# Kernel tuning notes

Hardware: AMD Instinct MI355X
Metric: run time of the kernel (lower is better)

The kernel has to match this reference:

```python
import jax, jax.numpy as jnp
import numpy as np

B, N, D = 4, 2048, 1024


def setup_inputs() -> dict:
    key = jax.random.key(0)
    ks = jax.random.split(key, 9)
    x = jax.random.normal(ks[0], (B, N, D), dtype=jnp.float32)
    # causal mask: True = masked (set to -inf), per dot_product_attention semantics
    mask = jnp.triu(jnp.ones((N, N), dtype=bool), k=1)
    mask = jnp.broadcast_to(mask, (B, N, N))
    scale = 1.0 / np.sqrt(D)
    Wq = jax.random.normal(ks[1], (D, D), dtype=jnp.float32) * scale
    Wk = jax.random.normal(ks[2], (D, D), dtype=jnp.float32) * scale
    Wv = jax.random.normal(ks[3], (D, D), dtype=jnp.float32) * scale
    Wo = jax.random.normal(ks[4], (D, D), dtype=jnp.float32) * scale
    bq = jnp.zeros((D,), dtype=jnp.float32)
    bk = jnp.zeros((D,), dtype=jnp.float32)
    bv = jnp.zeros((D,), dtype=jnp.float32)
    bo = jnp.zeros((D,), dtype=jnp.float32)
    return {"x": x, "mask": mask, "Wq": Wq, "bq": bq, "Wk": Wk, "bk": bk,
            "Wv": Wv, "bv": bv, "Wo": Wo, "bo": bo}


def reference(x, mask, Wq, bq, Wk, bk, Wv, bv, Wo, bo):
    # QKV projections (single-head despite docstring; module never splits heads)
    Q = x @ Wq + bq  # [b, n, d]
    K = x @ Wk + bk
    V = x @ Wv + bv
    d = K.shape[-1]
    scores = jnp.einsum('bqd,bkd->bqk', Q, K) / jnp.sqrt(jnp.asarray(d, Q.dtype))
    min_infty = jnp.finfo(scores.dtype).min
    scores = jnp.where(mask, min_infty, scores)
    weights = jax.nn.softmax(scores, axis=-1)
    attention = jnp.einsum('bqk,bkd->bqd', weights, V)
    out = attention @ Wo + bo
    return out
```

## Files before the change

kernel.cpp:

```cpp
#include <hip/hip_runtime.h>
#include <hip/hip_bf16.h>

typedef __attribute__((ext_vector_type(8))) short short8;
typedef __attribute__((ext_vector_type(4))) float f32x4;

__device__ inline float b2f(unsigned short u) {
    union { unsigned int i; float f; } c; c.i = ((unsigned int)u) << 16; return c.f;
}
__device__ inline unsigned short f2b(float f) {
    __hip_bfloat16 h = __float2bfloat16(f);
    return *reinterpret_cast<unsigned short*>(&h);
}

__device__ inline void gl_lds16(const unsigned short* g, unsigned short* ldsbase) {
    __builtin_amdgcn_global_load_lds(
        (const __attribute__((address_space(1))) unsigned int*)(g),
        (__attribute__((address_space(3))) unsigned int*)(ldsbase),
        16, 0, 0);
}

__global__ __launch_bounds__(256) void cvt_f32_bf16(
    const float* __restrict__ src, unsigned short* __restrict__ dst, int n4)
{
    int i = blockIdx.x * 256 + threadIdx.x;
    if (i >= n4) return;
    float4 v = ((const float4*)src)[i];
    union { unsigned short u[4]; unsigned long long ll; } p;
    p.u[0] = f2b(v.x); p.u[1] = f2b(v.y); p.u[2] = f2b(v.z); p.u[3] = f2b(v.w);
    ((unsigned long long*)dst)[i] = p.ll;
}

__global__ __launch_bounds__(256) void cvt_transpose(
    const float* __restrict__ src, unsigned short* __restrict__ dst, int R, int C)
{
    __shared__ float tile[32][33];
    const int c0 = blockIdx.x * 32, r0 = blockIdx.y * 32;
    const int tx = threadIdx.x & 31, ty = threadIdx.x >> 5;
    #pragma unroll
    for (int i = ty; i < 32; i += 8)
        tile[i][tx] = src[(long)(r0 + i) * C + c0 + tx];
    __syncthreads();
    #pragma unroll
    for (int i = ty; i < 32; i += 8)
        dst[(long)(c0 + i) * R + r0 + tx] = f2b(tile[tx][i]);
}


#define TILE_DECLS \
    __shared__ __attribute__((aligned(16))) unsigned short As[2 * 128 * 32]; \
    __shared__ __attribute__((aligned(16))) unsigned short Bs[2 * 128 * 32]; \
    const int t = threadIdx.x, lane = t & 63, w = t >> 6; \
    const int wr = w >> 1, wc = w & 1; \
    const int lrow = lane & 15, quad = lane >> 4; \
    f32x4 acc[4][4]; \
    _Pragma("unroll") for (int i = 0; i < 4; i++) \
        _Pragma("unroll") for (int j = 0; j < 4; j++) \
            acc[i][j] = (f32x4){0.f, 0.f, 0.f, 0.f};

#define TILE_KLOOP(gA, lda, gB, ldb, Keff) \
    for (int k0 = 0; k0 < (Keff); k0 += 64) { \
        _Pragma("unroll") for (int p = 0; p < 2; p++) \
            _Pragma("unroll") for (int h = 0; h < 2; h++) { \
                gl_lds16((gA) + (long)h * 16 * (lda) + k0 + p * 32, \
                         &As[p * 4096 + (w * 32 + h * 16) * 32]); \
                gl_lds16((gB) + (long)h * 16 * (ldb) + k0 + p * 32, \
                         &Bs[p * 4096 + (w * 32 + h * 16) * 32]); \
            } \
        __syncthreads(); \
        _Pragma("unroll") for (int p = 0; p < 2; p++) { \
            short8 af[4], bfr[4]; \
            _Pragma("unroll") for (int mi = 0; mi < 4; mi++) \
                af[mi] = *(const short8*)&As[p * 4096 + (wr * 64 + mi * 16 + lrow) * 32 + quad * 8]; \
            _Pragma("unroll") for (int ni = 0; ni < 4; ni++) \
                bfr[ni] = *(const short8*)&Bs[p * 4096 + (wc * 64 + ni * 16 + lrow) * 32 + quad * 8]; \
            _Pragma("unroll") for (int mi = 0; mi < 4; mi++) \
                _Pragma("unroll") for (int ni = 0; ni < 4; ni++) \
                    acc[mi][ni] = __builtin_amdgcn_mfma_f32_16x16x32_bf16( \
                        af[mi], bfr[ni], acc[mi][ni], 0, 0, 0); \
        } \
        __syncthreads(); \
    }

__global__ __launch_bounds__(256) void qkv_proj(
    const unsigned short* __restrict__ A,
    const unsigned short* __restrict__ Wqt, const unsigned short* __restrict__ Wkt,
    const unsigned short* __restrict__ Wvt,
    const float* __restrict__ bq, const float* __restrict__ bk, const float* __restrict__ bv,
    unsigned short* __restrict__ Q, unsigned short* __restrict__ Km,
    unsigned short* __restrict__ Vt)
{
    const int bm = blockIdx.x, bn = blockIdx.y;
    const int r = bn >> 3, bnn = bn & 7;
    const unsigned short* Bt = (r == 0) ? Wqt : (r == 1) ? Wkt : Wvt;
    const float* bias = (r == 0) ? bq : (r == 1) ? bk : bv;
    const int m0 = bm * 128, n0 = bnn * 128;

    TILE_DECLS

    const unsigned short* gA = A  + (long)(m0 + w * 32 + (lane >> 2)) * 1024 + (lane & 3) * 8;
    const unsigned short* gB = Bt + (long)(n0 + w * 32 + (lane >> 2)) * 1024 + (lane & 3) * 8;
    TILE_KLOOP(gA, 1024, gB, 1024, 1024)

    #pragma unroll
    for (int mi = 0; mi < 4; mi++) {
        const int m = m0 + wr * 64 + mi * 16 + quad * 4;
        #pragma unroll
        for (int ni = 0; ni < 4; ni++) {
            const int n = n0 + wc * 64 + ni * 16 + lrow;
            const float bvl = bias[n];
            if (r < 2) {
                unsigned short* out = (r == 0) ? Q : Km;
                #pragma unroll
                for (int rg = 0; rg < 4; rg++)
                    out[(long)(m + rg) * 1024 + n] = f2b(acc[mi][ni][rg] + bvl);
            } else {
                #pragma unroll
                for (int rg = 0; rg < 4; rg++)
                    Vt[(long)n * 8192 + m + rg] = f2b(acc[mi][ni][rg] + bvl);
            }
        }
    }
}

template<bool TRI, bool KCAUSAL, int OMODE>
__global__ __launch_bounds__(256) void gemm128(
    const unsigned short* __restrict__ A, const unsigned short* __restrict__ Bt,
    const float* __restrict__ bias, void* __restrict__ Cv,
    int K, int lda, int ldb, int ldc, long sA, long sB, long sC, float scale)
{
    int bm, bn, bz;
    if (TRI) {
        const int q = blockIdx.x;
        bm = (int)((sqrtf(8.f * q + 1.f) - 1.f) * 0.5f);
        while ((bm + 1) * (bm + 2) / 2 <= q) bm++;
        while (bm * (bm + 1) / 2 > q) bm--;
        bn = q - bm * (bm + 1) / 2;
        bz = blockIdx.y;
    } else {
        bm = blockIdx.x; bn = blockIdx.y; bz = blockIdx.z;
    }
    A  += (long)bz * sA;
    Bt += (long)bz * sB;
    const int m0 = bm * 128, n0 = bn * 128;

    TILE_DECLS

    const int Keff = KCAUSAL ? ((bm + 1) * 128 < K ? (bm + 1) * 128 : K) : K;
    const unsigned short* gA = A  + (long)(m0 + w * 32 + (lane >> 2)) * lda + (lane & 3) * 8;
    const unsigned short* gB = Bt + (long)(n0 + w * 32 + (lane >> 2)) * ldb + (lane & 3) * 8;
    TILE_KLOOP(gA, lda, gB, ldb, Keff)

    #pragma unroll
    for (int mi = 0; mi < 4; mi++) {
        const int m = m0 + wr * 64 + mi * 16 + quad * 4;
        #pragma unroll
        for (int ni = 0; ni < 4; ni++) {
            const int n = n0 + wc * 64 + ni * 16 + lrow;
            const float bvl = bias ? bias[n] : 0.f;
            #pragma unroll
            for (int rg = 0; rg < 4; rg++) {
                const float val = acc[mi][ni][rg] * scale + bvl;
                if (OMODE == 1)
                    ((float*)Cv)[(long)bz * sC + (long)(m + rg) * ldc + n] = val;
                else
                    ((unsigned short*)Cv)[(long)bz * sC + (long)(m + rg) * ldc + n] = f2b(val);
            }
        }
    }
}

__global__ __launch_bounds__(256) void softmax_causal(unsigned short* S, int Nseq)
{
    const long row = blockIdx.x;
    const int i = (int)(row % Nseq);
    unsigned short* base = S + row * (long)Nseq;
    const int len = i + 1;
    const int t = threadIdx.x;

    __shared__ float smax[4], ssum[4];

    float lmax = -3.0e38f;
    for (int j = t; j < len; j += 256) lmax = fmaxf(lmax, b2f(base[j]));
    #pragma unroll
    for (int off = 32; off > 0; off >>= 1) lmax = fmaxf(lmax, __shfl_xor(lmax, off, 64));
    if ((t & 63) == 0) smax[t >> 6] = lmax;
    __syncthreads();
    const float gmax = fmaxf(fmaxf(smax[0], smax[1]), fmaxf(smax[2], smax[3]));

    float lsum = 0.f;
    for (int j = t; j < len; j += 256) lsum += __expf(b2f(base[j]) - gmax);
    #pragma unroll
    for (int off = 32; off > 0; off >>= 1) lsum += __shfl_xor(lsum, off, 64);
    if ((t & 63) == 0) ssum[t >> 6] = lsum;
    __syncthreads();
    const float inv = 1.0f / (ssum[0] + ssum[1] + ssum[2] + ssum[3]);

    const int padded = ((i >> 7) + 1) << 7;
    for (int j = t; j < padded; j += 256) {
        const float v = (j < len) ? __expf(b2f(base[j]) - gmax) * inv : 0.f;
        base[j] = f2b(v);
    }
}

extern "C" void kernel_launch(void* const* d_in, const int* in_sizes, int n_in,
                              void* d_out, int out_size, void* d_ws, size_t ws_size,
                              hipStream_t stream)
{
    const float* x  = (const float*)d_in[0];
    const float* Wq = (const float*)d_in[2];
    const float* bq = (const float*)d_in[3];
    const float* Wk = (const float*)d_in[4];
    const float* bk = (const float*)d_in[5];
    const float* Wv = (const float*)d_in[6];
    const float* bv = (const float*)d_in[7];
    const float* Wo = (const float*)d_in[8];
    const float* bo = (const float*)d_in[9];

    unsigned short* ws = (unsigned short*)d_ws;
    const long XSZ = 8192L * 1024;
    const long WSZ = 1024L * 1024;
    unsigned short* xb  = ws;
    unsigned short* Wqt = ws + XSZ;
    unsigned short* Wkt = Wqt + WSZ;
    unsigned short* Wvt = Wkt + WSZ;
    unsigned short* Wot = Wvt + WSZ;
    unsigned short* Q   = Wot + WSZ;
    unsigned short* Km  = Q + XSZ;
    unsigned short* Vt  = Km + XSZ;
    unsigned short* S   = Vt + XSZ;
    unsigned short* Aat = xb;

    const dim3 blk(256);

    cvt_f32_bf16 <<<dim3(8192), blk, 0, stream>>>(x, xb, (int)(XSZ / 4));
    cvt_transpose<<<dim3(32, 32), blk, 0, stream>>>(Wq, Wqt, 1024, 1024);
    cvt_transpose<<<dim3(32, 32), blk, 0, stream>>>(Wk, Wkt, 1024, 1024);
    cvt_transpose<<<dim3(32, 32), blk, 0, stream>>>(Wv, Wvt, 1024, 1024);
    cvt_transpose<<<dim3(32, 32), blk, 0, stream>>>(Wo, Wot, 1024, 1024);

    qkv_proj<<<dim3(64, 24), blk, 0, stream>>>(
        xb, Wqt, Wkt, Wvt, bq, bk, bv, Q, Km, Vt);

    gemm128<true, false, 0><<<dim3(136, 4), blk, 0, stream>>>(
        Q, Km, nullptr, S, 1024, 1024, 1024, 2048,
        2048L * 1024, 2048L * 1024, 2048L * 2048, 0.03125f);

    softmax_causal<<<dim3(4 * 2048), blk, 0, stream>>>(S, 2048);

    gemm128<false, true, 0><<<dim3(16, 8, 4), blk, 0, stream>>>(
        S, Vt, nullptr, Aat, 2048, 2048, 8192, 1024,
        2048L * 2048, 2048, 2048L * 1024, 1.f);

    gemm128<false, false, 1><<<dim3(64, 8, 1), blk, 0, stream>>>(
        Aat, Wot, bo, (float*)d_out, 1024, 1024, 1024, 1024, 0, 0, 0, 1.f);
}
```

Baseline: 358.5 us.

## Fold output projection into V weights and vectorize causal softmax

```diff
diff --git a/kernel.cpp b/kernel.cpp
--- a/kernel.cpp
+++ b/kernel.cpp
@@ -30,21 +30,33 @@
     ((unsigned long long*)dst)[i] = p.ll;
 }
 
-__global__ __launch_bounds__(256) void cvt_transpose(
-    const float* __restrict__ src, unsigned short* __restrict__ dst, int R, int C)
-{
+__global__ __launch_bounds__(256) void cvt_transpose3(
+    const float* __restrict__ s0, const float* __restrict__ s1, const float* __restrict__ s2,
+    unsigned short* __restrict__ d0, unsigned short* __restrict__ d1, unsigned short* __restrict__ d2)
+{
+    const float* src = blockIdx.z == 0 ? s0 : blockIdx.z == 1 ? s1 : s2;
+    unsigned short* dst = blockIdx.z == 0 ? d0 : blockIdx.z == 1 ? d1 : d2;
     __shared__ float tile[32][33];
     const int c0 = blockIdx.x * 32, r0 = blockIdx.y * 32;
     const int tx = threadIdx.x & 31, ty = threadIdx.x >> 5;
     #pragma unroll
     for (int i = ty; i < 32; i += 8)
-        tile[i][tx] = src[(long)(r0 + i) * C + c0 + tx];
+        tile[i][tx] = src[(long)(r0 + i) * 1024 + c0 + tx];
     __syncthreads();
     #pragma unroll
     for (int i = ty; i < 32; i += 8)
-        dst[(long)(c0 + i) * R + r0 + tx] = f2b(tile[tx][i]);
-}
-
+        dst[(long)(c0 + i) * 1024 + r0 + tx] = f2b(tile[tx][i]);
+}
+
+__global__ __launch_bounds__(256) void make_bvo(
+    const float* __restrict__ Wo, const float* __restrict__ bv,
+    const float* __restrict__ bo, float* __restrict__ bvo)
+{
+    const int n = blockIdx.x * 256 + threadIdx.x;
+    float acc = bo[n];
+    for (int k = 0; k < 1024; k++) acc += bv[k] * Wo[(long)k * 1024 + n];
+    bvo[n] = acc;
+}
 
 #define TILE_DECLS \
     __shared__ __attribute__((aligned(16))) unsigned short As[2 * 128 * 32]; \
@@ -84,15 +96,15 @@
 __global__ __launch_bounds__(256) void qkv_proj(
     const unsigned short* __restrict__ A,
     const unsigned short* __restrict__ Wqt, const unsigned short* __restrict__ Wkt,
-    const unsigned short* __restrict__ Wvt,
-    const float* __restrict__ bq, const float* __restrict__ bk, const float* __restrict__ bv,
+    const unsigned short* __restrict__ Wvot,
+    const float* __restrict__ bq, const float* __restrict__ bk,
     unsigned short* __restrict__ Q, unsigned short* __restrict__ Km,
-    unsigned short* __restrict__ Vt)
+    unsigned short* __restrict__ Vot)
 {
     const int bm = blockIdx.x, bn = blockIdx.y;
     const int r = bn >> 3, bnn = bn & 7;
-    const unsigned short* Bt = (r == 0) ? Wqt : (r == 1) ? Wkt : Wvt;
-    const float* bias = (r == 0) ? bq : (r == 1) ? bk : bv;
+    const unsigned short* Bt = (r == 0) ? Wqt : (r == 1) ? Wkt : Wvot;
+    const float* bias = (r == 0) ? bq : (r == 1) ? bk : nullptr;
     const int m0 = bm * 128, n0 = bnn * 128;
 
     TILE_DECLS
@@ -107,7 +119,7 @@
         #pragma unroll
         for (int ni = 0; ni < 4; ni++) {
             const int n = n0 + wc * 64 + ni * 16 + lrow;
-            const float bvl = bias[n];
+            const float bvl = bias ? bias[n] : 0.f;
             if (r < 2) {
                 unsigned short* out = (r == 0) ? Q : Km;
                 #pragma unroll
@@ -116,7 +128,7 @@
             } else {
                 #pragma unroll
                 for (int rg = 0; rg < 4; rg++)
-                    Vt[(long)n * 8192 + m + rg] = f2b(acc[mi][ni][rg] + bvl);
+                    Vot[(long)n * 8192 + m + rg] = f2b(acc[mi][ni][rg]);
             }
         }
     }
@@ -169,36 +181,56 @@
     }
 }
 
-__global__ __launch_bounds__(256) void softmax_causal(unsigned short* S, int Nseq)
+__global__ __launch_bounds__(256) void softmax_causal(unsigned short* __restrict__ S)
 {
     const long row = blockIdx.x;
-    const int i = (int)(row % Nseq);
-    unsigned short* base = S + row * (long)Nseq;
-    const int len = i + 1;
+    const int i = (int)(row & 2047);
+    unsigned short* base = S + row * 2048;
     const int t = threadIdx.x;
-
-    __shared__ float smax[4], ssum[4];
-
-    float lmax = -3.0e38f;
-    for (int j = t; j < len; j += 256) lmax = fmaxf(lmax, b2f(base[j]));
+    const int padded = ((i >> 7) + 1) << 7;
+    const int j0 = t * 8;
+    const bool active = j0 < padded;
+
+    __shared__ float red[4];
+
+    float v[8];
+    if (active) {
+        short8 s8 = *(const short8*)(base + j0);
+        #pragma unroll
+        for (int jj = 0; jj < 8; jj++)
+            v[jj] = (j0 + jj <= i) ? b2f((unsigned short)s8[jj]) : -3.0e38f;
+    } else {
+        #pragma unroll
+        for (int jj = 0; jj < 8; jj++) v[jj] = -3.0e38f;
+    }
+
+    float lmax = v[0];
+    #pragma unroll
+    for (int jj = 1; jj < 8; jj++) lmax = fmaxf(lmax, v[jj]);
     #pragma unroll
     for (int off = 32; off > 0; off >>= 1) lmax = fmaxf(lmax, __shfl_xor(lmax, off, 64));
-    if ((t & 63) == 0) smax[t >> 6] = lmax;
-    __syncthreads();
-    const float gmax = fmaxf(fmaxf(smax[0], smax[1]), fmaxf(smax[2], smax[3]));
+    if ((t & 63) == 0) red[t >> 6] = lmax;
+    __syncthreads();
+    const float gmax = fmaxf(fmaxf(red[0], red[1]), fmaxf(red[2], red[3]));
+    __syncthreads();
 
     float lsum = 0.f;
-    for (int j = t; j < len; j += 256) lsum += __expf(b2f(base[j]) - gmax);
+    #pragma unroll
+    for (int jj = 0; jj < 8; jj++) {
+        v[jj] = (v[jj] > -1.0e37f) ? __expf(v[jj] - gmax) : 0.f;
+        lsum += v[jj];
+    }
     #pragma unroll
     for (int off = 32; off > 0; off >>= 1) lsum += __shfl_xor(lsum, off, 64);
-    if ((t & 63) == 0) ssum[t >> 6] = lsum;
-    __syncthreads();
-    const float inv = 1.0f / (ssum[0] + ssum[1] + ssum[2] + ssum[3]);
-
-    const int padded = ((i >> 7) + 1) << 7;
-    for (int j = t; j < padded; j += 256) {
-        const float v = (j < len) ? __expf(b2f(base[j]) - gmax) * inv : 0.f;
-        base[j] = f2b(v);
+    if ((t & 63) == 0) red[t >> 6] = lsum;
+    __syncthreads();
+    const float inv = 1.0f / (red[0] + red[1] + red[2] + red[3]);
+
+    if (active) {
+        short8 p8;
+        #pragma unroll
+        for (int jj = 0; jj < 8; jj++) p8[jj] = (short)f2b(v[jj] * inv);
+        *(short8*)(base + j0) = p8;
     }
 }
 
@@ -219,38 +251,38 @@
     unsigned short* ws = (unsigned short*)d_ws;
     const long XSZ = 8192L * 1024;
     const long WSZ = 1024L * 1024;
-    unsigned short* xb  = ws;
-    unsigned short* Wqt = ws + XSZ;
-    unsigned short* Wkt = Wqt + WSZ;
-    unsigned short* Wvt = Wkt + WSZ;
-    unsigned short* Wot = Wvt + WSZ;
-    unsigned short* Q   = Wot + WSZ;
-    unsigned short* Km  = Q + XSZ;
-    unsigned short* Vt  = Km + XSZ;
-    unsigned short* S   = Vt + XSZ;
-    unsigned short* Aat = xb;
+    unsigned short* xb   = ws;
+    unsigned short* Wqt  = ws + XSZ;
+    unsigned short* Wkt  = Wqt + WSZ;
+    unsigned short* Wot  = Wkt + WSZ;
+    unsigned short* Wvb  = Wot + WSZ;
+    unsigned short* Wvot = Wvb + WSZ;
+    unsigned short* Q    = Wvot + WSZ;
+    unsigned short* Km   = Q + XSZ;
+    unsigned short* Vot  = Km + XSZ;
+    unsigned short* S    = Vot + XSZ;
+    float*          bvo  = (float*)(S + 4L * 2048 * 2048);
 
     const dim3 blk(256);
 
-    cvt_f32_bf16 <<<dim3(8192), blk, 0, stream>>>(x, xb, (int)(XSZ / 4));
-    cvt_transpose<<<dim3(32, 32), blk, 0, stream>>>(Wq, Wqt, 1024, 1024);
-    cvt_transpose<<<dim3(32, 32), blk, 0, stream>>>(Wk, Wkt, 1024, 1024);
-    cvt_transpose<<<dim3(32, 32), blk, 0, stream>>>(Wv, Wvt, 1024, 1024);
-    cvt_transpose<<<dim3(32, 32), blk, 0, stream>>>(Wo, Wot, 1024, 1024);
+    cvt_f32_bf16  <<<dim3(8192), blk, 0, stream>>>(x, xb, (int)(XSZ / 4));
+    cvt_f32_bf16  <<<dim3(1024), blk, 0, stream>>>(Wv, Wvb, (int)(WSZ / 4));
+    cvt_transpose3<<<dim3(32, 32, 3), blk, 0, stream>>>(Wq, Wk, Wo, Wqt, Wkt, Wot);
+    make_bvo      <<<dim3(4), blk, 0, stream>>>(Wo, bv, bo, bvo);
+
+    gemm128<false, false, 0><<<dim3(8, 8, 1), blk, 0, stream>>>(
+        Wot, Wvb, nullptr, Wvot, 1024, 1024, 1024, 1024, 0, 0, 0, 1.f);
 
     qkv_proj<<<dim3(64, 24), blk, 0, stream>>>(
-        xb, Wqt, Wkt, Wvt, bq, bk, bv, Q, Km, Vt);
+        xb, Wqt, Wkt, Wvot, bq, bk, Q, Km, Vot);
 
     gemm128<true, false, 0><<<dim3(136, 4), blk, 0, stream>>>(
         Q, Km, nullptr, S, 1024, 1024, 1024, 2048,
         2048L * 1024, 2048L * 1024, 2048L * 2048, 0.03125f);
 
-    softmax_causal<<<dim3(4 * 2048), blk, 0, stream>>>(S, 2048);
-
-    gemm128<false, true, 0><<<dim3(16, 8, 4), blk, 0, stream>>>(
-        S, Vt, nullptr, Aat, 2048, 2048, 8192, 1024,
+    softmax_causal<<<dim3(4 * 2048), blk, 0, stream>>>(S);
+
+    gemm128<false, true, 1><<<dim3(16, 8, 4), blk, 0, stream>>>(
+        S, Vot, bvo, (float*)d_out, 2048, 2048, 8192, 1024,
         2048L * 2048, 2048, 2048L * 1024, 1.f);
-
-    gemm128<false, false, 1><<<dim3(64, 8, 1), blk, 0, stream>>>(
-        Aat, Wot, bo, (float*)d_out, 1024, 1024, 1024, 1024, 0, 0, 0, 1.f);
-}
+}
```

After: 371.9 us. 3.8% more time.
